# Performance work log

Measured on AMD Instinct MI355X. Metric: run time of the kernel, lower is better.

Reference implementation:

```python
import jax, jax.numpy as jnp
import numpy as np

T, N = 8192, 1024
W_MEAN, W_VAR = 0.2, 0.4


def setup_inputs() -> dict:
    key = jax.random.key(0)
    k_x, k_w = jax.random.split(key, 2)
    x_in = jax.random.normal(k_x, (T, N), dtype=jnp.float32) * 5.0
    # w ~ U(w_mean - w_var, w_mean + w_var), matching the torch init
    w = W_MEAN - W_VAR + 2.0 * W_VAR * jax.random.uniform(k_w, (N, N), dtype=jnp.float32)
    ones = jnp.ones((N,), jnp.float32)
    return {
        "x_in": x_in,
        "w": w,
        "E_L": -54.0 * ones,
        "tau_m": 1.4 * ones,
        "G": 0.7 * ones,
        "R_I": 132.0 * ones,
        "f_v": 0.3 * ones,
        "f_I": 0.6 * ones,
        "delta_theta_s": 11.0 * ones,
        "b_s": 0.3 * ones,
        "a_v": 0.3 * ones,
        "b_v": 0.3 * ones,
        "theta_inf": -24.5 * ones,
        "delta_V": 10.0 * ones,
        "I_A": 1.6 * ones,
    }


def reference(x_in, w, E_L, tau_m, G, R_I, f_v, f_I, delta_theta_s, b_s,
              a_v, b_v, theta_inf, delta_V, I_A):
    n = w.shape[0]
    # self_recurrence_mask = ones(N,N) - eye(N)
    w_masked = w * (1.0 - jnp.eye(n, dtype=w.dtype))

    def step(carry, x):
        v, theta_s, theta_v, I_add = carry
        I = I_add @ w_masked + 0.85 * x  # [N] recurrent drive + scaled input
        v_next = v + (I * R_I - G * (v - E_L)) / tau_m
        thr = theta_s + theta_v
        spiked_soft = jax.nn.sigmoid(v_next - thr)  # surrogate spike (self.spiked)
        spiked = (v_next >= thr).astype(v.dtype)    # hard spike
        not_spiked = 1.0 - spiked
        v_reset = E_L + f_v * (v - E_L) - delta_V
        v_new = spiked * v_reset + not_spiked * v_next
        theta_s_new = (1.0 - b_s) * theta_s + spiked * delta_theta_s
        d_theta_v = a_v * (v_new - E_L) - b_v * (theta_v - theta_inf)
        theta_v_new = theta_v + not_spiked * d_theta_v
        I_add_new = (1.0 - f_I) * I_add + spiked_soft * I_A
        return (v_new, theta_s_new, theta_v_new, I_add_new), (v_new, spiked_soft)

    init = (E_L,                               # v = E_L * ones(N)
            30.0 * jnp.ones_like(E_L),         # theta_s
            jnp.ones_like(E_L),                # theta_v
            jnp.zeros_like(E_L))               # I_additive
    _, (vs, spikes) = jax.lax.scan(step, init, x_in)
    return vs, spikes  # each [T, N]
```

## Files before the change

kernel.cpp:

```cpp
#include <hip/hip_runtime.h>


#define T_STEPS 8192
#define N_NEUR  1024
#define NBLK    32
#define COLS    32
#define TPB     256

__global__ void glif_init(unsigned long long* __restrict__ buf) {
    int i = blockIdx.x * blockDim.x + threadIdx.x;
    if (i < N_NEUR) {
        buf[i] = 0ULL;
    } else if (i < 2 * N_NEUR) {
        buf[i] = 0xFFFFFFFF00000000ULL;
    }
}

__launch_bounds__(TPB, 1)
__global__ void glif_main(const float* __restrict__ x_in,
                          const float* __restrict__ w,
                          const float* __restrict__ E_L_p,
                          const float* __restrict__ tau_m_p,
                          const float* __restrict__ G_p,
                          const float* __restrict__ R_I_p,
                          const float* __restrict__ f_v_p,
                          const float* __restrict__ f_I_p,
                          const float* __restrict__ dths_p,
                          const float* __restrict__ b_s_p,
                          const float* __restrict__ a_v_p,
                          const float* __restrict__ b_v_p,
                          const float* __restrict__ th_inf_p,
                          const float* __restrict__ dV_p,
                          const float* __restrict__ I_A_p,
                          float* __restrict__ out,
                          unsigned long long* __restrict__ buf) {
    const int tid  = threadIdx.x;
    const int wv   = tid >> 6;
    const int lane = tid & 63;
    const int half = lane >> 5;
    const int colL = lane & 31;
    const int colG = blockIdx.x * COLS + colL;
    const int ibase = wv * 256 + half * 128;

    __shared__ float ix[N_NEUR];
    __shared__ float red[4 * 32];

    float wreg[128];
#pragma unroll
    for (int k = 0; k < 128; ++k) {
        int i = ibase + k;
        float v = w[(size_t)i * N_NEUR + colG];
        wreg[k] = (i == colG) ? 0.0f : v;
    }

    const bool owner = (wv == 0) && (lane < 32);
    float E_L = 0.f, inv_tau = 0.f, Gc = 0.f, R_I = 0.f, f_v = 0.f, f_I = 0.f;
    float dths = 0.f, b_s = 0.f, a_v = 0.f, b_v = 0.f, th_inf = 0.f, dV = 0.f, I_A = 0.f;
    float v = 0.f, th_s = 0.f, th_v = 0.f, I_own = 0.f, xnext = 0.f;
    if (owner) {
        E_L     = E_L_p[colG];
        inv_tau = 1.0f / tau_m_p[colG];
        Gc      = G_p[colG];
        R_I     = R_I_p[colG];
        f_v     = f_v_p[colG];
        f_I     = f_I_p[colG];
        dths    = dths_p[colG];
        b_s     = b_s_p[colG];
        a_v     = a_v_p[colG];
        b_v     = b_v_p[colG];
        th_inf  = th_inf_p[colG];
        dV      = dV_p[colG];
        I_A     = I_A_p[colG];
        v = E_L; th_s = 30.0f; th_v = 1.0f; I_own = 0.0f;
        xnext = x_in[colG];
    }

    float* __restrict__ vs_out = out;
    float* __restrict__ sp_out = out + (size_t)T_STEPS * N_NEUR;

    for (int t = 0; t < T_STEPS; ++t) {
        {
            unsigned long long* src = buf + (size_t)(t & 1) * N_NEUR + tid * 4;
            float4 vals;
            unsigned got = 0;
            while (got != 0xFu) {
#pragma unroll
                for (int k = 0; k < 4; ++k) {
                    if (!(got & (1u << k))) {
                        unsigned long long u = __hip_atomic_load(
                            src + k, __ATOMIC_RELAXED, __HIP_MEMORY_SCOPE_AGENT);
                        if ((unsigned)(u >> 32) == (unsigned)t) {
                            (&vals.x)[k] = __uint_as_float((unsigned)(u & 0xFFFFFFFFu));
                            got |= (1u << k);
                        }
                    }
                }
            }
            ((float4*)ix)[tid] = vals;
        }
        float xt = xnext;
        if (owner) {
            int tn = (t + 1 < T_STEPS) ? (t + 1) : t;
            xnext = x_in[(size_t)tn * N_NEUR + colG];
        }
        __syncthreads();

        float acc = 0.0f;
        const float4* ixv = (const float4*)(ix + ibase);
#pragma unroll
        for (int k = 0; k < 32; ++k) {
            float4 q = ixv[k];
            acc = fmaf(wreg[4 * k + 0], q.x, acc);
            acc = fmaf(wreg[4 * k + 1], q.y, acc);
            acc = fmaf(wreg[4 * k + 2], q.z, acc);
            acc = fmaf(wreg[4 * k + 3], q.w, acc);
        }
        acc += __shfl_xor(acc, 32, 64);
        if (lane < 32) red[wv * 32 + lane] = acc;
        __syncthreads();

        if (owner) {
            float I = red[colL] + red[32 + colL] + red[64 + colL] + red[96 + colL]
                      + 0.85f * xt;
            float v_next = v + (I * R_I - Gc * (v - E_L)) * inv_tau;
            float thr = th_s + th_v;
            float z = v_next - thr;
            float soft = 1.0f / (1.0f + __expf(-z));
            bool  sp = (v_next >= thr);
            float v_reset = E_L + f_v * (v - E_L) - dV;
            float v_new = sp ? v_reset : v_next;
            th_s = (1.0f - b_s) * th_s + (sp ? dths : 0.0f);
            float d_thv = a_v * (v_new - E_L) - b_v * (th_v - th_inf);
            th_v = th_v + (sp ? 0.0f : d_thv);
            I_own = (1.0f - f_I) * I_own + soft * I_A;
            v = v_new;

            vs_out[(size_t)t * N_NEUR + colG] = v_new;
            sp_out[(size_t)t * N_NEUR + colG] = soft;

            unsigned long long pk =
                ((unsigned long long)(unsigned)(t + 1) << 32) |
                (unsigned long long)__float_as_uint(I_own);
            __hip_atomic_store(buf + (size_t)((t + 1) & 1) * N_NEUR + colG, pk,
                               __ATOMIC_RELAXED, __HIP_MEMORY_SCOPE_AGENT);
        }
    }
}

extern "C" void kernel_launch(void* const* d_in, const int* in_sizes, int n_in,
                              void* d_out, int out_size, void* d_ws, size_t ws_size,
                              hipStream_t stream) {
    const float* x_in   = (const float*)d_in[0];
    const float* w      = (const float*)d_in[1];
    const float* E_L    = (const float*)d_in[2];
    const float* tau_m  = (const float*)d_in[3];
    const float* G      = (const float*)d_in[4];
    const float* R_I    = (const float*)d_in[5];
    const float* f_v    = (const float*)d_in[6];
    const float* f_I    = (const float*)d_in[7];
    const float* dths   = (const float*)d_in[8];
    const float* b_s    = (const float*)d_in[9];
    const float* a_v    = (const float*)d_in[10];
    const float* b_v    = (const float*)d_in[11];
    const float* th_inf = (const float*)d_in[12];
    const float* dV     = (const float*)d_in[13];
    const float* I_A    = (const float*)d_in[14];

    float* out = (float*)d_out;
    unsigned long long* buf = (unsigned long long*)d_ws;

    glif_init<<<(2 * N_NEUR + TPB - 1) / TPB, TPB, 0, stream>>>(buf);
    glif_main<<<NBLK, TPB, 0, stream>>>(x_in, w, E_L, tau_m, G, R_I, f_v, f_I,
                                        dths, b_s, a_v, b_v, th_inf, dV, I_A,
                                        out, buf);
}
```

Measured before the change: 17.79 ms.

## Use single-wavefront blocks across 128 CUs with shuffle-only reduction

Repartitions the persistent recurrent kernel from 32 blocks of 256 threads to 128 single-wave blocks, each owning 8 columns split across 8 row chunks. The cross-wave shared-memory reduction and both __syncthreads are replaced by intra-wave shuffles, and a swizzled LDS layout is used to avoid bank conflicts. The aim is to shorten the serial per-timestep critical path and spread the weight matrix over more CUs. In exchange, 128 blocks must now spin on the global flag buffer each step, which adds more polling traffic on the atomic flags.

```diff
diff --git a/kernel.cpp b/kernel.cpp
--- a/kernel.cpp
+++ b/kernel.cpp
@@ -3,9 +3,8 @@
 
 #define T_STEPS 8192
 #define N_NEUR  1024
-#define NBLK    32
-#define COLS    32
-#define TPB     256
+#define NBLK    128
+#define TPB     64
 
 __global__ void glif_init(unsigned long long* __restrict__ buf) {
     int i = blockIdx.x * blockDim.x + threadIdx.x;
@@ -34,114 +33,108 @@
                           const float* __restrict__ I_A_p,
                           float* __restrict__ out,
                           unsigned long long* __restrict__ buf) {
-    const int tid  = threadIdx.x;
-    const int wv   = tid >> 6;
-    const int lane = tid & 63;
-    const int half = lane >> 5;
-    const int colL = lane & 31;
-    const int colG = blockIdx.x * COLS + colL;
-    const int ibase = wv * 256 + half * 128;
+    const int lane = threadIdx.x;
+    const int rc   = lane >> 3;
+    const int cl   = lane & 7;
+    const int col  = blockIdx.x * 8 + cl;
 
-    __shared__ float ix[N_NEUR];
-    __shared__ float red[4 * 32];
+    __shared__ float4 ix[256];
 
     float wreg[128];
 #pragma unroll
-    for (int k = 0; k < 128; ++k) {
-        int i = ibase + k;
-        float v = w[(size_t)i * N_NEUR + colG];
-        wreg[k] = (i == colG) ? 0.0f : v;
+    for (int j = 0; j < 128; ++j) {
+        int r = rc * 128 + j;
+        float wv = w[(size_t)r * N_NEUR + col];
+        wreg[j] = (r == col) ? 0.0f : wv;
     }
 
-    const bool owner = (wv == 0) && (lane < 32);
-    float E_L = 0.f, inv_tau = 0.f, Gc = 0.f, R_I = 0.f, f_v = 0.f, f_I = 0.f;
-    float dths = 0.f, b_s = 0.f, a_v = 0.f, b_v = 0.f, th_inf = 0.f, dV = 0.f, I_A = 0.f;
-    float v = 0.f, th_s = 0.f, th_v = 0.f, I_own = 0.f, xnext = 0.f;
-    if (owner) {
-        E_L     = E_L_p[colG];
-        inv_tau = 1.0f / tau_m_p[colG];
-        Gc      = G_p[colG];
-        R_I     = R_I_p[colG];
-        f_v     = f_v_p[colG];
-        f_I     = f_I_p[colG];
-        dths    = dths_p[colG];
-        b_s     = b_s_p[colG];
-        a_v     = a_v_p[colG];
-        b_v     = b_v_p[colG];
-        th_inf  = th_inf_p[colG];
-        dV      = dV_p[colG];
-        I_A     = I_A_p[colG];
-        v = E_L; th_s = 30.0f; th_v = 1.0f; I_own = 0.0f;
-        xnext = x_in[colG];
-    }
+    const float E_L    = E_L_p[col];
+    const float inv_tau = 1.0f / tau_m_p[col];
+    const float Gc     = G_p[col];
+    const float R_I    = R_I_p[col];
+    const float f_v    = f_v_p[col];
+    const float om_fI  = 1.0f - f_I_p[col];
+    const float dths   = dths_p[col];
+    const float om_bs  = 1.0f - b_s_p[col];
+    const float a_v    = a_v_p[col];
+    const float b_v    = b_v_p[col];
+    const float th_inf = th_inf_p[col];
+    const float dV     = dV_p[col];
+    const float I_A    = I_A_p[col];
+
+    float v = E_L, th_s = 30.0f, th_v = 1.0f, I_own = 0.0f;
+    float xnext = x_in[col];
 
     float* __restrict__ vs_out = out;
     float* __restrict__ sp_out = out + (size_t)T_STEPS * N_NEUR;
 
     for (int t = 0; t < T_STEPS; ++t) {
-        {
-            unsigned long long* src = buf + (size_t)(t & 1) * N_NEUR + tid * 4;
-            float4 vals;
-            unsigned got = 0;
-            while (got != 0xFu) {
+        unsigned long long* src = buf + (size_t)(t & 1) * N_NEUR + lane * 16;
+        float vals[16];
+        unsigned got = 0;
+        while (got != 0xFFFFu) {
 #pragma unroll
-                for (int k = 0; k < 4; ++k) {
-                    if (!(got & (1u << k))) {
-                        unsigned long long u = __hip_atomic_load(
-                            src + k, __ATOMIC_RELAXED, __HIP_MEMORY_SCOPE_AGENT);
-                        if ((unsigned)(u >> 32) == (unsigned)t) {
-                            (&vals.x)[k] = __uint_as_float((unsigned)(u & 0xFFFFFFFFu));
-                            got |= (1u << k);
-                        }
+            for (int k = 0; k < 16; ++k) {
+                if (!(got & (1u << k))) {
+                    unsigned long long u = __hip_atomic_load(
+                        src + k, __ATOMIC_RELAXED, __HIP_MEMORY_SCOPE_AGENT);
+                    if ((unsigned)(u >> 32) == (unsigned)t) {
+                        vals[k] = __uint_as_float((unsigned)(u & 0xFFFFFFFFu));
+                        got |= (1u << k);
                     }
                 }
             }
-            ((float4*)ix)[tid] = vals;
+        }
+
+#pragma unroll
+        for (int i = 0; i < 4; ++i) {
+            int c = 4 * lane + i;
+            int p = c ^ ((c >> 5) & 7);
+            ix[p] = make_float4(vals[4*i], vals[4*i+1], vals[4*i+2], vals[4*i+3]);
         }
         float xt = xnext;
-        if (owner) {
+        {
             int tn = (t + 1 < T_STEPS) ? (t + 1) : t;
-            xnext = x_in[(size_t)tn * N_NEUR + colG];
+            xnext = x_in[(size_t)tn * N_NEUR + col];
         }
-        __syncthreads();
+        asm volatile("s_waitcnt lgkmcnt(0)" ::: "memory");
+        __builtin_amdgcn_sched_barrier(0);
 
-        float acc = 0.0f;
-        const float4* ixv = (const float4*)(ix + ibase);
+        float a0 = 0.f, a1 = 0.f, a2 = 0.f, a3 = 0.f;
 #pragma unroll
-        for (int k = 0; k < 32; ++k) {
-            float4 q = ixv[k];
-            acc = fmaf(wreg[4 * k + 0], q.x, acc);
-            acc = fmaf(wreg[4 * k + 1], q.y, acc);
-            acc = fmaf(wreg[4 * k + 2], q.z, acc);
-            acc = fmaf(wreg[4 * k + 3], q.w, acc);
+        for (int m = 0; m < 32; ++m) {
+            float4 q = ix[rc * 32 + (m ^ rc)];
+            a0 = fmaf(wreg[4*m+0], q.x, a0);
+            a1 = fmaf(wreg[4*m+1], q.y, a1);
+            a2 = fmaf(wreg[4*m+2], q.z, a2);
+            a3 = fmaf(wreg[4*m+3], q.w, a3);
         }
+        float acc = (a0 + a1) + (a2 + a3);
+        acc += __shfl_xor(acc, 8, 64);
+        acc += __shfl_xor(acc, 16, 64);
         acc += __shfl_xor(acc, 32, 64);
-        if (lane < 32) red[wv * 32 + lane] = acc;
-        __syncthreads();
 
-        if (owner) {
-            float I = red[colL] + red[32 + colL] + red[64 + colL] + red[96 + colL]
-                      + 0.85f * xt;
-            float v_next = v + (I * R_I - Gc * (v - E_L)) * inv_tau;
-            float thr = th_s + th_v;
-            float z = v_next - thr;
-            float soft = 1.0f / (1.0f + __expf(-z));
-            bool  sp = (v_next >= thr);
-            float v_reset = E_L + f_v * (v - E_L) - dV;
-            float v_new = sp ? v_reset : v_next;
-            th_s = (1.0f - b_s) * th_s + (sp ? dths : 0.0f);
-            float d_thv = a_v * (v_new - E_L) - b_v * (th_v - th_inf);
-            th_v = th_v + (sp ? 0.0f : d_thv);
-            I_own = (1.0f - f_I) * I_own + soft * I_A;
-            v = v_new;
+        float I = acc + 0.85f * xt;
+        float v_next = v + (I * R_I - Gc * (v - E_L)) * inv_tau;
+        float thr = th_s + th_v;
+        float z = v_next - thr;
+        float soft = 1.0f / (1.0f + __expf(-z));
+        bool  sp = (v_next >= thr);
+        float v_reset = E_L + f_v * (v - E_L) - dV;
+        float v_new = sp ? v_reset : v_next;
+        th_s = om_bs * th_s + (sp ? dths : 0.0f);
+        float d_thv = a_v * (v_new - E_L) - b_v * (th_v - th_inf);
+        th_v = th_v + (sp ? 0.0f : d_thv);
+        I_own = om_fI * I_own + soft * I_A;
+        v = v_new;
 
-            vs_out[(size_t)t * N_NEUR + colG] = v_new;
-            sp_out[(size_t)t * N_NEUR + colG] = soft;
-
+        if (rc == 0) {
+            __builtin_nontemporal_store(v_new, &vs_out[(size_t)t * N_NEUR + col]);
+            __builtin_nontemporal_store(soft, &sp_out[(size_t)t * N_NEUR + col]);
             unsigned long long pk =
                 ((unsigned long long)(unsigned)(t + 1) << 32) |
                 (unsigned long long)__float_as_uint(I_own);
-            __hip_atomic_store(buf + (size_t)((t + 1) & 1) * N_NEUR + colG, pk,
+            __hip_atomic_store(buf + (size_t)((t + 1) & 1) * N_NEUR + col, pk,
                                __ATOMIC_RELAXED, __HIP_MEMORY_SCOPE_AGENT);
         }
     }
@@ -169,7 +162,7 @@
     float* out = (float*)d_out;
     unsigned long long* buf = (unsigned long long*)d_ws;
 
-    glif_init<<<(2 * N_NEUR + TPB - 1) / TPB, TPB, 0, stream>>>(buf);
+    glif_init<<<8, 256, 0, stream>>>(buf);
     glif_main<<<NBLK, TPB, 0, stream>>>(x_in, w, E_L, tau_m, G, R_I, f_v, f_I,
                                         dths, b_s, a_v, b_v, th_inf, dV, I_A,
                                         out, buf);
```

Result: slower. 35.76 ms (+101.1%).
